# Kernel optimization log

Measured on AMD Instinct MI355X. Metric: run time of the kernel, lower is better.

## Reference

```python
import jax, jax.numpy as jnp
import numpy as np
from jax import lax

K = 32768          # queue size
C = 100            # num_classes == len(cls_num_list1)
B = 1024           # batch size (features.shape[0] - K)
D = 128            # embedding dim
ALPHA = 0.05; BETA = 1.0; GAMMA = 1.0; SUPT = 1.0
T = 0.07; BASE_T = 0.07   # base_temperature defaults to temperature
SMOOTH = 0.0; EPS = 1e-12


def setup_inputs() -> dict:
    key = jax.random.key(0)
    k1, k2, k3, k4 = jax.random.split(key, 4)
    features = jax.random.normal(k1, (B + K, D), dtype=jnp.float32)
    features = features / jnp.linalg.norm(features, axis=1, keepdims=True)  # contrastive feats are L2-normalized
    centers = jax.random.normal(k2, (C, D), dtype=jnp.float32)
    centers = centers / jnp.linalg.norm(centers, axis=1, keepdims=True)
    sup_logits = jax.random.normal(k3, (B, C), dtype=jnp.float32)
    labels = jax.random.randint(k4, (B + K,), 0, C, dtype=jnp.int32)
    return {"features": features, "sup_logits": sup_logits, "centers": centers, "labels": labels}


def _loss(features, sup_logits, centers, labels):
    f32 = features.dtype
    lab_c = jnp.arange(C, dtype=labels.dtype)
    lab1 = jnp.concatenate([labels[:B], lab_c])                 # [B+C]
    mask = (labels[:B, None] == labels[None, :]).astype(f32)    # [B, B+K]
    mask1 = (lab1[:B, None] == lab1[None, :]).astype(f32)       # [B, B+C]
    # class counts over batch+queue (batch_cls_count) and batch+centers (batch_cls_count1)
    cls_count = jnp.zeros((C,), f32).at[labels].add(1.0)
    cls_count1 = jnp.zeros((C,), f32).at[lab1].add(1.0)
    diag = jnp.arange(B)
    logits_mask = jnp.ones((B, B + K), f32).at[diag, diag].set(0.0)
    logits_mask1 = jnp.ones((B, B + C), f32).at[diag, diag].set(0.0)
    mask = mask * logits_mask
    mask1 = mask1 * logits_mask1

    # ---- branch 1: batch anchors vs [batch, class centers] ----
    feats1 = jnp.concatenate([features[:B], centers], axis=0)   # [B+C, D]
    logits1 = (features[:B] @ feats1.T) / T                     # [B, B+C]
    logits1 = logits1 - lax.stop_gradient(logits1.max(axis=1, keepdims=True))
    exp1 = jnp.exp(logits1) * logits_mask1
    w1 = cls_count1[lab1][None, :] - mask1                      # per-instance class weight
    denom1 = (exp1 / w1).sum(axis=1, keepdims=True)
    log_prob1 = logits1 - jnp.log(denom1 + EPS)
    loss1 = -jnp.mean((mask1 * log_prob1).sum(1) / mask1.sum(1))

    # ---- branch 2: [sup_logits, batch anchors vs batch+queue] ----
    adc = (features[:B] @ features.T) / T                       # [B, B+K]
    logits = jnp.concatenate([sup_logits / SUPT, adc], axis=1)  # [B, C+B+K] (self.weight is None)
    logits = logits - lax.stop_gradient(logits.max(axis=1, keepdims=True))
    one_hot = jax.nn.one_hot(labels[:B], C, dtype=f32)
    one_hot = SMOOTH / (C - 1) * (1.0 - one_hot) + (1.0 - SMOOTH) * one_hot
    mask_full = jnp.concatenate([one_hot * BETA, mask * ALPHA], axis=1)
    lmask_full = jnp.concatenate([jnp.ones((B, C), f32), GAMMA * logits_mask], axis=1)
    expl = jnp.exp(logits) * lmask_full
    lab_full = jnp.concatenate([lab_c, labels])                 # [C+B+K]
    w = cls_count[lab_full][None, :] - mask_full
    denom = (expl / w).sum(axis=1, keepdims=True)
    log_prob = logits - jnp.log(denom + EPS)
    loss2 = -(T / BASE_T) * jnp.mean((mask_full * log_prob).sum(1) / mask_full.sum(1))
    return loss1 + loss2


def reference(features, sup_logits, centers, labels):
    return _loss(features, sup_logits, centers, labels)
```

## Files before the change

### kernel.cpp

```cpp
#include <hip/hip_runtime.h>
#include <math.h>

#define KQ   32768
#define CC   100
#define BB   1024
#define DD   128
#define NTOT (BB + KQ)
#define CB_CENT 1056
#define NCB  1060
#define NHIST 33
#define NCG2 132
#define CG_SUP 141
#define NSL  141

#define INV_T  14.285714285714286f
#define K2E    20.609929f
#define ALPHA  0.05f
#define EPSV   1e-12f

typedef __attribute__((ext_vector_type(8)))  short          short8;
typedef __attribute__((ext_vector_type(8)))  unsigned short ushort8;
typedef __attribute__((ext_vector_type(16))) float          float16;

__device__ __forceinline__ unsigned short f2bf_rne(float f) {
    unsigned int u = __float_as_uint(f);
    return (unsigned short)((u + 0x7FFFu + ((u >> 16) & 1u)) >> 16);
}


__global__ __launch_bounds__(256) void prep_k(const float* __restrict__ feats,
                                              const float* __restrict__ centers,
                                              const int* __restrict__ labels,
                                              unsigned short* __restrict__ X2,
                                              int* __restrict__ cntP,
                                              int* __restrict__ cntB) {
    const int b = blockIdx.x, t = threadIdx.x;
    if (b >= NCB) {
        const int h = b - NCB;
        __shared__ int hA[CC], hB[CC];
        if (t < CC) { hA[t] = 0; hB[t] = 0; }
        __syncthreads();
        const int base = h * 1024;
#pragma unroll
        for (int q = 0; q < 4; ++q) {
            int l = labels[base + q * 256 + t];
            atomicAdd(&hA[l], 1);
            if (h == 0) atomicAdd(&hB[l], 1);
        }
        __syncthreads();
        if (t < 128) {
            cntP[h * 128 + t] = (t < CC) ? hA[t] : 0;
            if (h == 0) cntB[t] = (t < CC) ? hB[t] : 0;
        }
        return;
    }
    __shared__ unsigned short sm[8 * 66 * 8];
    const int cb = b;
    const int rl = t >> 3, c8 = t & 7;
    const int r = cb * 32 + rl;
    const float* src;
    if (r < NTOT)            src = &feats[(size_t)r * DD];
    else if (r < NTOT + CC)  src = &centers[(size_t)(r - NTOT) * DD];
    else                     src = nullptr;
#pragma unroll
    for (int s = 0; s < 2; ++s) {
        const int c8p = c8 + 8 * s;
        float v[8];
        if (src) {
            const float4* p = (const float4*)(src + c8p * 8);
            float4 q0 = p[0], q1 = p[1];
            v[0]=q0.x; v[1]=q0.y; v[2]=q0.z; v[3]=q0.w;
            v[4]=q1.x; v[5]=q1.y; v[6]=q1.z; v[7]=q1.w;
        } else {
#pragma unroll
            for (int j = 0; j < 8; ++j) v[j] = 0.f;
        }
        ushort8 H;
#pragma unroll
        for (int m = 0; m < 8; ++m) H[m] = f2bf_rne(v[m]);
        const int ks = c8p >> 1, lh = c8p & 1;
        *(ushort8*)&sm[(ks * 66 + rl + 32 * lh) * 8] = H;
    }
    __syncthreads();
    ushort8* dst = (ushort8*)((char*)X2 + (size_t)cb * 8192);
#pragma unroll
    for (int j = 0; j < 2; ++j) {
        const int idx = j * 256 + t;
        const int ks = idx >> 6, ln2 = idx & 63;
        dst[idx] = *(const ushort8*)&sm[(ks * 66 + ln2) * 8];
    }
}

__global__ __launch_bounds__(128) void tables_k(
    const int* __restrict__ cntP, const int* __restrict__ cntB,
    float2* __restrict__ wA, float2* __restrict__ w1, float2* __restrict__ wS,
    float* __restrict__ cAf, int* __restrict__ cBi) {
    const int t = threadIdx.x;
    int s = 0;
#pragma unroll
    for (int h = 0; h < NHIST; ++h) s += cntP[h * 128 + t];
    float cf = (float)s;
    float rn = (s > 0) ? __builtin_amdgcn_rcpf(cf) : 0.f;
    float dr = (s > 0) ? (__builtin_amdgcn_rcpf(cf - ALPHA) - rn) : 0.f;
    wA[t] = make_float2(rn, dr);
    wS[t] = make_float2(__builtin_amdgcn_rcpf(cf),
                        __builtin_amdgcn_rcpf(fmaxf(cf - 1.f, 1.f)));
    int sb = cntB[t];
    float c1 = (float)(sb + 1);
    float r1 = __builtin_amdgcn_rcpf(c1);
    w1[t] = make_float2(r1, __builtin_amdgcn_rcpf(fmaxf(c1 - 1.f, 1.f)) - r1);
    cAf[t] = cf;
    cBi[t] = sb;
}

__device__ __forceinline__ void epi_tile(
    const float16& acc, int cb, int lc, float rn, float drm, bool checkDiag,
    int half, int ln, int growbase, const int* rlab, float* sS, float* sN)
{
    const int ccol = cb * 32 + ln;
#pragma unroll
    for (int reg = 0; reg < 16; ++reg) {
        int ro = (reg & 3) + 8 * (reg >> 2) + 4 * half;
        float a  = acc[reg];
        float mf = (lc == rlab[reg]) ? 1.f : 0.f;
        float wgt = fmaf(mf, drm, rn);
        if (checkDiag) {
            bool d = (ccol == growbase + ro);
            wgt = d ? 0.f : wgt;
            mf  = d ? 0.f : mf;
        }
        float e = exp2f(fmaf(a, K2E, -K2E));
        sS[reg] = fmaf(e, wgt, sS[reg]);
        sN[reg] = fmaf(mf, a, sN[reg]);
    }
}

__global__ __launch_bounds__(256, 2) void gemm_k(
    const unsigned short* __restrict__ X2, const int* __restrict__ labels,
    const float2* __restrict__ wA, const float2* __restrict__ w1,
    const float2* __restrict__ wS, const float* __restrict__ sup,
    float* __restrict__ pS, float* __restrict__ pN,
    float* __restrict__ supS, float* __restrict__ supLi) {
    const int b = blockIdx.x;
    const int xcd = b & 7, rgrp = (b >> 3) & 7, chunk = b >> 6;
    const int cg = chunk * 8 + xcd;
    if (cg > CG_SUP) return;

    const int tid = threadIdx.x;
    const int w = tid >> 6, lane = tid & 63;
    const int half = lane >> 5, ln = lane & 31;
    const int rb = rgrp * 4 + w;
    const char* Xb = (const char*)X2;

    if (cg == CG_SUP) {
        const int c0 = lane, c1 = lane + 64;
        float2 t0 = wS[c0];
        float rA0 = t0.x, rAm0 = t0.y;
        float rA1 = 0.f, rAm1 = 0.f;
        if (lane < 36) { float2 t1v = wS[c1]; rA1 = t1v.x; rAm1 = t1v.y; }
        for (int rr = 0; rr < 32; ++rr) {
            int row = rb * 32 + rr;
            int li = labels[row];
            const float* srow = &sup[(size_t)row * CC];
            float v0 = srow[c0];
            float s = __expf(v0 - INV_T) * ((c0 == li) ? rAm0 : rA0);
            float liv = (c0 == li) ? v0 : 0.f;
            if (lane < 36) {
                float v1 = srow[c1];
                s += __expf(v1 - INV_T) * ((c1 == li) ? rAm1 : rA1);
                liv += (c1 == li) ? v1 : 0.f;
            }
#pragma unroll
            for (int off = 1; off < 64; off <<= 1) {
                s += __shfl_xor(s, off, 64);
                liv += __shfl_xor(liv, off, 64);
            }
            if (lane == 0) { supS[row] = s; supLi[row] = liv; }
        }
        return;
    }

    __shared__ char sm[2 * 8192];
    __shared__ float2 wT[128];

    const bool isB2 = (cg < NCG2);
    const int t1 = cg - NCG2;
    const bool isBatch = isB2 || (t1 < 8);
    const int NIT = isB2 ? 8 : 4;
    const int cb0 = isB2 ? cg * 8 : (t1 < 8 ? t1 * 4 : CB_CENT);

    if (tid < 128) wT[tid] = isB2 ? wA[tid] : w1[tid];
    __syncthreads();

    int lcv[8];
#pragma unroll
    for (int i = 0; i < 8; ++i) {
        if (i < NIT) {
            const int cb = cb0 + i;
            if (isBatch) {
                lcv[i] = labels[cb * 32 + ln];
            } else {
                int q = cb * 32 + ln - NTOT;
                lcv[i] = (q < CC) ? q : -1;
            }
        } else lcv[i] = -1;
    }

    const int growbase = rb * 32;
    short8 Ah[8];
    {
        size_t abase = (size_t)rb * 8192 + (size_t)lane * 16;
#pragma unroll
        for (int ks = 0; ks < 8; ++ks)
            Ah[ks] = *(const short8*)(Xb + abase + (size_t)ks * 1024);
    }
    int rlab[16];
#pragma unroll
    for (int reg = 0; reg < 16; ++reg) {
        int ro = (reg & 3) + 8 * (reg >> 2) + 4 * half;
        rlab[reg] = labels[growbase + ro];
    }

    float rnv[8], drv[8];
#pragma unroll
    for (int i = 0; i < 8; ++i) {
        if (i < NIT) {
            int lc = lcv[i];
            float2 wv = wT[(lc >= 0) ? lc : 0];
            rnv[i] = (lc >= 0) ? wv.x : 0.f;
            drv[i] = (lc >= 0) ? wv.y : 0.f;
        } else { rnv[i] = 0.f; drv[i] = 0.f; }
    }

    float sS[16], sN[16];
#pragma unroll
    for (int reg = 0; reg < 16; ++reg) { sS[reg] = 0.f; sN[reg] = 0.f; }

    const int soff = (w * 2) * 1024 + lane * 16;

    {
        const char* src = Xb + (size_t)cb0 * 8192 + soff;
        short8 s0 = *(const short8*)src;
        short8 s1 = *(const short8*)(src + 1024);
        *(short8*)&sm[soff] = s0;
        *(short8*)&sm[soff + 1024] = s1;
    }
    __syncthreads();

    for (int i = 0; i < NIT; ++i) {
        const int cb = cb0 + i;
        short8 st0, st1;
        const bool more = (i + 1 < NIT);
        if (more) {
            const char* src = Xb + (size_t)(cb + 1) * 8192 + soff;
            st0 = *(const short8*)src;
            st1 = *(const short8*)(src + 1024);
        }
        const char* Bp = &sm[(i & 1) * 8192 + lane * 16];
        float16 a;
#pragma unroll
        for (int reg = 0; reg < 16; ++reg) a[reg] = 0.f;
#pragma unroll
        for (int ks = 0; ks < 8; ++ks) {
            short8 Bf = *(const short8*)(Bp + ks * 1024);
            a = __builtin_amdgcn_mfma_f32_32x32x16_bf16(Ah[ks], Bf, a, 0, 0, 0);
        }
        epi_tile(a, cb, lcv[i], rnv[i], drv[i], isBatch && (cb == rb),
                 half, ln, growbase, rlab, sS, sN);
        if (more) {
            char* d = &sm[((i + 1) & 1) * 8192 + soff];
            *(short8*)d = st0;
            *(short8*)(d + 1024) = st1;
        }
        __syncthreads();
    }

    const int slice = isB2 ? cg : (NCG2 + t1);
#pragma unroll
    for (int reg = 0; reg < 16; ++reg) {
        float av = sS[reg], c = sN[reg];
#pragma unroll
        for (int off = 1; off < 32; off <<= 1) {
            av += __shfl_xor(av, off, 64);
            c  += __shfl_xor(c, off, 64);
        }
        if (ln == 0) {
            int ro = (reg & 3) + 8 * (reg >> 2) + 4 * half;
            int grow = growbase + ro;
            pS[(size_t)slice * BB + grow] = av;
            pN[(size_t)slice * BB + grow] = c;
        }
    }
}

__global__ __launch_bounds__(256) void reduce_k(
    const int* __restrict__ labels,
    const float* __restrict__ cAf, const int* __restrict__ cBi,
    const float* __restrict__ pS, const float* __restrict__ pN,
    const float* __restrict__ supS, const float* __restrict__ supLi,
    float* __restrict__ partial) {
    const int g = blockIdx.x, t = threadIdx.x;
    const int rl = t >> 5, j = t & 31;
    const int row = g * 8 + rl;
    float S2 = 0.f, N2 = 0.f, S1 = 0.f, N1v = 0.f;
    for (int c = j; c < NCG2; c += 32) {
        S2 += pS[(size_t)c * BB + row];
        N2 += pN[(size_t)c * BB + row];
    }
    if (NCG2 + j < NSL) {
        S1  += pS[(size_t)(NCG2 + j) * BB + row];
        N1v += pN[(size_t)(NCG2 + j) * BB + row];
    }
#pragma unroll
    for (int off = 1; off < 32; off <<= 1) {
        S2 += __shfl_xor(S2, off, 64);  N2  += __shfl_xor(N2, off, 64);
        S1 += __shfl_xor(S1, off, 64);  N1v += __shfl_xor(N1v, off, 64);
    }
    float s = 0.f;
    if (j == 0) {
        int li = labels[row];
        S2 += supS[row];
        N2 *= INV_T; N1v *= INV_T;
        float sli = supLi[row];
        float cA = cAf[li];
        float msum2 = fmaf(ALPHA, cA - 1.f, 1.f);
        float loss2 = -(fmaf(ALPHA, N2, sli) / msum2 - INV_T - logf(S2 + EPSV));
        float loss1 = -(N1v / (float)cBi[li] - INV_T - logf(S1 + EPSV));
        s = loss1 + loss2;
    }
#pragma unroll
    for (int off = 1; off < 64; off <<= 1) s += __shfl_xor(s, off, 64);
    __shared__ float buf[4];
    if ((t & 63) == 0) buf[t >> 6] = s;
    __syncthreads();
    if (t == 0) partial[g] = (buf[0] + buf[1]) + (buf[2] + buf[3]);
}

__global__ __launch_bounds__(64) void final_k(const float* __restrict__ partial,
                                              float* __restrict__ out) {
    const int t = threadIdx.x;
    float s = partial[t] + partial[t + 64];
#pragma unroll
    for (int off = 1; off < 64; off <<= 1) s += __shfl_xor(s, off, 64);
    if (t == 0) out[0] = s / (float)BB;
}

extern "C" void kernel_launch(void* const* d_in, const int* in_sizes, int n_in,
                              void* d_out, int out_size, void* d_ws, size_t ws_size,
                              hipStream_t stream) {
    const float* feats   = (const float*)d_in[0];
    const float* sup     = (const float*)d_in[1];
    const float* centers = (const float*)d_in[2];
    const int*   labels  = (const int*)d_in[3];
    float* out = (float*)d_out;
    char*  wsb = (char*)d_ws;

    const size_t X2_BYTES = (size_t)NCB * 8192;
    unsigned short* X2 = (unsigned short*)wsb;
    char* base2 = wsb + X2_BYTES;
    int* cntP = (int*)base2;
    int* cntB = cntP + NHIST * 128;
    float2* wA = (float2*)(cntB + 128);
    float2* w1 = wA + 128;
    float2* wS = w1 + 128;
    float*  cAf = (float*)(wS + 128);
    int*    cBi = (int*)(cAf + 128);
    float* pS = (float*)(cBi + 128);
    float* pN = pS + (size_t)NSL * BB;
    float* supS  = pN + (size_t)NSL * BB;
    float* supLi = supS + BB;
    float* partial = supLi + BB;

    prep_k<<<NCB + NHIST, 256, 0, stream>>>(feats, centers, labels, X2, cntP, cntB);
    tables_k<<<1, 128, 0, stream>>>(cntP, cntB, wA, w1, wS, cAf, cBi);
    gemm_k<<<18 * 64, 256, 0, stream>>>(X2, labels, wA, w1, wS, sup,
                                        pS, pN, supS, supLi);
    reduce_k<<<128, 256, 0, stream>>>(labels, cAf, cBi, pS, pN, supS, supLi, partial);
    final_k<<<1, 64, 0, stream>>>(partial, out);
}
```

Baseline: 121.5 us.

## Give each wave two 32-row A tiles to double reuse of staged B tiles

Each wave now holds two 32-row anchor blocks in registers and runs two MFMA chains against every shared-memory column tile, so each block covers 256 rows and the grid shrinks from 1152 to 576 blocks. The aim is to halve how often the queue feature tiles are loaded from global memory and copied into LDS. The cost is roughly double the register footprint (A fragments, accumulators, label and sum arrays) under launch_bounds(256,2), which can cause spills or lower occupancy, and there are half as many blocks to spread across CUs. The sup-logit path is rescaled to 64 rows per wave to match the new grid.

After: 153.8 us. 1.27x slower.

```diff
diff --git a/kernel.cpp b/kernel.cpp
--- a/kernel.cpp
+++ b/kernel.cpp
@@ -142,14 +142,13 @@
     float* __restrict__ pS, float* __restrict__ pN,
     float* __restrict__ supS, float* __restrict__ supLi) {
     const int b = blockIdx.x;
-    const int xcd = b & 7, rgrp = (b >> 3) & 7, chunk = b >> 6;
+    const int xcd = b & 7, rgrp = (b >> 3) & 3, chunk = b >> 5;
     const int cg = chunk * 8 + xcd;
     if (cg > CG_SUP) return;
 
     const int tid = threadIdx.x;
     const int w = tid >> 6, lane = tid & 63;
     const int half = lane >> 5, ln = lane & 31;
-    const int rb = rgrp * 4 + w;
     const char* Xb = (const char*)X2;
 
     if (cg == CG_SUP) {
@@ -158,8 +157,9 @@
         float rA0 = t0.x, rAm0 = t0.y;
         float rA1 = 0.f, rAm1 = 0.f;
         if (lane < 36) { float2 t1v = wS[c1]; rA1 = t1v.x; rAm1 = t1v.y; }
-        for (int rr = 0; rr < 32; ++rr) {
-            int row = rb * 32 + rr;
+        const int rbase = rgrp * 256 + w * 64;
+        for (int rr = 0; rr < 64; ++rr) {
+            int row = rbase + rr;
             int li = labels[row];
             const float* srow = &sup[(size_t)row * CC];
             float v0 = srow[c0];
@@ -190,7 +190,9 @@
     const int cb0 = isB2 ? cg * 8 : (t1 < 8 ? t1 * 4 : CB_CENT);
 
     if (tid < 128) wT[tid] = isB2 ? wA[tid] : w1[tid];
-    __syncthreads();
+
+    const int rb0 = rgrp * 8 + w * 2, rb1 = rb0 + 1;
+    const int growb0 = rb0 * 32, growb1 = rb1 * 32;
 
     int lcv[8];
 #pragma unroll
@@ -206,35 +208,29 @@
         } else lcv[i] = -1;
     }
 
-    const int growbase = rb * 32;
-    short8 Ah[8];
+    short8 Ah0[8], Ah1[8];
     {
-        size_t abase = (size_t)rb * 8192 + (size_t)lane * 16;
-#pragma unroll
-        for (int ks = 0; ks < 8; ++ks)
-            Ah[ks] = *(const short8*)(Xb + abase + (size_t)ks * 1024);
-    }
-    int rlab[16];
+        size_t a0 = (size_t)rb0 * 8192 + (size_t)lane * 16;
+        size_t a1 = (size_t)rb1 * 8192 + (size_t)lane * 16;
+#pragma unroll
+        for (int ks = 0; ks < 8; ++ks) {
+            Ah0[ks] = *(const short8*)(Xb + a0 + (size_t)ks * 1024);
+            Ah1[ks] = *(const short8*)(Xb + a1 + (size_t)ks * 1024);
+        }
+    }
+    int rlab0[16], rlab1[16];
 #pragma unroll
     for (int reg = 0; reg < 16; ++reg) {
         int ro = (reg & 3) + 8 * (reg >> 2) + 4 * half;
-        rlab[reg] = labels[growbase + ro];
-    }
-
-    float rnv[8], drv[8];
-#pragma unroll
-    for (int i = 0; i < 8; ++i) {
-        if (i < NIT) {
-            int lc = lcv[i];
-            float2 wv = wT[(lc >= 0) ? lc : 0];
-            rnv[i] = (lc >= 0) ? wv.x : 0.f;
-            drv[i] = (lc >= 0) ? wv.y : 0.f;
-        } else { rnv[i] = 0.f; drv[i] = 0.f; }
-    }
-
-    float sS[16], sN[16];
-#pragma unroll
-    for (int reg = 0; reg < 16; ++reg) { sS[reg] = 0.f; sN[reg] = 0.f; }
+        rlab0[reg] = labels[growb0 + ro];
+        rlab1[reg] = labels[growb1 + ro];
+    }
+
+    float sS0[16], sN0[16], sS1[16], sN1[16];
+#pragma unroll
+    for (int reg = 0; reg < 16; ++reg) {
+        sS0[reg] = 0.f; sN0[reg] = 0.f; sS1[reg] = 0.f; sN1[reg] = 0.f;
+    }
 
     const int soff = (w * 2) * 1024 + lane * 16;
 
@@ -256,17 +252,24 @@
             st0 = *(const short8*)src;
             st1 = *(const short8*)(src + 1024);
         }
+        int lc = lcv[i];
+        float2 wv = wT[(lc >= 0) ? lc : 0];
+        float rn  = (lc >= 0) ? wv.x : 0.f;
+        float drm = (lc >= 0) ? wv.y : 0.f;
         const char* Bp = &sm[(i & 1) * 8192 + lane * 16];
-        float16 a;
-#pragma unroll
-        for (int reg = 0; reg < 16; ++reg) a[reg] = 0.f;
+        float16 a0, a1;
+#pragma unroll
+        for (int reg = 0; reg < 16; ++reg) { a0[reg] = 0.f; a1[reg] = 0.f; }
 #pragma unroll
         for (int ks = 0; ks < 8; ++ks) {
             short8 Bf = *(const short8*)(Bp + ks * 1024);
-            a = __builtin_amdgcn_mfma_f32_32x32x16_bf16(Ah[ks], Bf, a, 0, 0, 0);
-        }
-        epi_tile(a, cb, lcv[i], rnv[i], drv[i], isBatch && (cb == rb),
-                 half, ln, growbase, rlab, sS, sN);
+            a0 = __builtin_amdgcn_mfma_f32_32x32x16_bf16(Ah0[ks], Bf, a0, 0, 0, 0);
+            a1 = __builtin_amdgcn_mfma_f32_32x32x16_bf16(Ah1[ks], Bf, a1, 0, 0, 0);
+        }
+        epi_tile(a0, cb, lc, rn, drm, isBatch && (cb == rb0),
+                 half, ln, growb0, rlab0, sS0, sN0);
+        epi_tile(a1, cb, lc, rn, drm, isBatch && (cb == rb1),
+                 half, ln, growb1, rlab1, sS1, sN1);
         if (more) {
             char* d = &sm[((i + 1) & 1) * 8192 + soff];
             *(short8*)d = st0;
@@ -278,17 +281,21 @@
     const int slice = isB2 ? cg : (NCG2 + t1);
 #pragma unroll
     for (int reg = 0; reg < 16; ++reg) {
-        float av = sS[reg], c = sN[reg];
+        float av0 = sS0[reg], c0v = sN0[reg];
+        float av1 = sS1[reg], c1v = sN1[reg];
 #pragma unroll
         for (int off = 1; off < 32; off <<= 1) {
-            av += __shfl_xor(av, off, 64);
-            c  += __shfl_xor(c, off, 64);
+            av0 += __shfl_xor(av0, off, 64);
+            c0v += __shfl_xor(c0v, off, 64);
+            av1 += __shfl_xor(av1, off, 64);
+            c1v += __shfl_xor(c1v, off, 64);
         }
         if (ln == 0) {
             int ro = (reg & 3) + 8 * (reg >> 2) + 4 * half;
-            int grow = growbase + ro;
-            pS[(size_t)slice * BB + grow] = av;
-            pN[(size_t)slice * BB + grow] = c;
+            pS[(size_t)slice * BB + growb0 + ro] = av0;
+            pN[(size_t)slice * BB + growb0 + ro] = c0v;
+            pS[(size_t)slice * BB + growb1 + ro] = av1;
+            pN[(size_t)slice * BB + growb1 + ro] = c1v;
         }
     }
 }
@@ -373,7 +380,7 @@
 
     prep_k<<<NCB + NHIST, 256, 0, stream>>>(feats, centers, labels, X2, cntP, cntB);
     tables_k<<<1, 128, 0, stream>>>(cntP, cntB, wA, w1, wS, cAf, cBi);
-    gemm_k<<<18 * 64, 256, 0, stream>>>(X2, labels, wA, w1, wS, sup,
+    gemm_k<<<18 * 32, 256, 0, stream>>>(X2, labels, wA, w1, wS, sup,
                                         pS, pN, supS, supLi);
     reduce_k<<<128, 256, 0, stream>>>(labels, cAf, cBi, pS, pN, supS, supLi, partial);
     final_k<<<1, 64, 0, stream>>>(partial, out);
```

## Fold tables kernel into gemm/reduce and stage B tiles via global_load_lds

Applied to the files above, without the earlier changes.

Removes the single-block tables_k launch by having each gemm and reduce block recompute the class-count weight tables from the histogram partials. Replaces the register-staged global-to-LDS double-buffer copy with direct global_load_lds async loads, so the prefetch no longer holds VGPRs or needs explicit LDS stores. This saves one kernel launch and serialization gap, at the cost of redundant histogram summation in every block. It also relies on the async LDS writes being complete before the barrier without an explicit vmcnt wait.

New measurement: 121.1 us. No clear change (-0.3%).

```diff
diff --git a/kernel.cpp b/kernel.cpp
--- a/kernel.cpp
+++ b/kernel.cpp
@@ -25,6 +25,12 @@
 __device__ __forceinline__ unsigned short f2bf_rne(float f) {
     unsigned int u = __float_as_uint(f);
     return (unsigned short)((u + 0x7FFFu + ((u >> 16) & 1u)) >> 16);
+}
+
+__device__ __forceinline__ void glds16(const void* g, void* l) {
+    __builtin_amdgcn_global_load_lds(
+        (const __attribute__((address_space(1))) void*)g,
+        (__attribute__((address_space(3))) void*)l, 16, 0, 0);
 }
 
 
@@ -91,28 +97,6 @@
     }
 }
 
-__global__ __launch_bounds__(128) void tables_k(
-    const int* __restrict__ cntP, const int* __restrict__ cntB,
-    float2* __restrict__ wA, float2* __restrict__ w1, float2* __restrict__ wS,
-    float* __restrict__ cAf, int* __restrict__ cBi) {
-    const int t = threadIdx.x;
-    int s = 0;
-#pragma unroll
-    for (int h = 0; h < NHIST; ++h) s += cntP[h * 128 + t];
-    float cf = (float)s;
-    float rn = (s > 0) ? __builtin_amdgcn_rcpf(cf) : 0.f;
-    float dr = (s > 0) ? (__builtin_amdgcn_rcpf(cf - ALPHA) - rn) : 0.f;
-    wA[t] = make_float2(rn, dr);
-    wS[t] = make_float2(__builtin_amdgcn_rcpf(cf),
-                        __builtin_amdgcn_rcpf(fmaxf(cf - 1.f, 1.f)));
-    int sb = cntB[t];
-    float c1 = (float)(sb + 1);
-    float r1 = __builtin_amdgcn_rcpf(c1);
-    w1[t] = make_float2(r1, __builtin_amdgcn_rcpf(fmaxf(c1 - 1.f, 1.f)) - r1);
-    cAf[t] = cf;
-    cBi[t] = sb;
-}
-
 __device__ __forceinline__ void epi_tile(
     const float16& acc, int cb, int lc, float rn, float drm, bool checkDiag,
     int half, int ln, int growbase, const int* rlab, float* sS, float* sN)
@@ -137,8 +121,8 @@
 
 __global__ __launch_bounds__(256, 2) void gemm_k(
     const unsigned short* __restrict__ X2, const int* __restrict__ labels,
-    const float2* __restrict__ wA, const float2* __restrict__ w1,
-    const float2* __restrict__ wS, const float* __restrict__ sup,
+    const int* __restrict__ cntP, const int* __restrict__ cntB,
+    const float* __restrict__ sup,
     float* __restrict__ pS, float* __restrict__ pN,
     float* __restrict__ supS, float* __restrict__ supLi) {
     const int b = blockIdx.x;
@@ -154,10 +138,21 @@
 
     if (cg == CG_SUP) {
         const int c0 = lane, c1 = lane + 64;
-        float2 t0 = wS[c0];
-        float rA0 = t0.x, rAm0 = t0.y;
+        int s0 = 0, s1 = 0;
+#pragma unroll
+        for (int h = 0; h < NHIST; ++h) {
+            s0 += cntP[h * 128 + c0];
+            s1 += cntP[h * 128 + c1];
+        }
+        float n0 = (float)s0;
+        float rA0 = __builtin_amdgcn_rcpf(n0);
+        float rAm0 = __builtin_amdgcn_rcpf(fmaxf(n0 - 1.f, 1.f));
         float rA1 = 0.f, rAm1 = 0.f;
-        if (lane < 36) { float2 t1v = wS[c1]; rA1 = t1v.x; rAm1 = t1v.y; }
+        if (lane < 36) {
+            float n1 = (float)s1;
+            rA1 = __builtin_amdgcn_rcpf(n1);
+            rAm1 = __builtin_amdgcn_rcpf(fmaxf(n1 - 1.f, 1.f));
+        }
         for (int rr = 0; rr < 32; ++rr) {
             int row = rb * 32 + rr;
             int li = labels[row];
@@ -189,8 +184,29 @@
     const int NIT = isB2 ? 8 : 4;
     const int cb0 = isB2 ? cg * 8 : (t1 < 8 ? t1 * 4 : CB_CENT);
 
-    if (tid < 128) wT[tid] = isB2 ? wA[tid] : w1[tid];
-    __syncthreads();
+    if (tid < 128) {
+        int s = 0;
+#pragma unroll
+        for (int h = 0; h < NHIST; ++h) s += cntP[h * 128 + tid];
+        float2 wv;
+        if (isB2) {
+            float cf = (float)s;
+            float rn = (s > 0) ? __builtin_amdgcn_rcpf(cf) : 0.f;
+            wv = make_float2(rn, (s > 0) ? (__builtin_amdgcn_rcpf(cf - ALPHA) - rn) : 0.f);
+        } else {
+            float c1 = (float)(cntB[tid] + 1);
+            float r1 = __builtin_amdgcn_rcpf(c1);
+            wv = make_float2(r1, __builtin_amdgcn_rcpf(fmaxf(c1 - 1.f, 1.f)) - r1);
+        }
+        wT[tid] = wv;
+    }
+
+    const int wbase = w * 2048;
+    {
+        const char* src = Xb + (size_t)cb0 * 8192 + wbase + lane * 16;
+        glds16(src, &sm[wbase]);
+        glds16(src + 1024, &sm[wbase + 1024]);
+    }
 
     int lcv[8];
 #pragma unroll
@@ -221,6 +237,8 @@
         rlab[reg] = labels[growbase + ro];
     }
 
+    __syncthreads();
+
     float rnv[8], drv[8];
 #pragma unroll
     for (int i = 0; i < 8; ++i) {
@@ -236,25 +254,14 @@
 #pragma unroll
     for (int reg = 0; reg < 16; ++reg) { sS[reg] = 0.f; sN[reg] = 0.f; }
 
-    const int soff = (w * 2) * 1024 + lane * 16;
-
-    {
-        const char* src = Xb + (size_t)cb0 * 8192 + soff;
-        short8 s0 = *(const short8*)src;
-        short8 s1 = *(const short8*)(src + 1024);
-        *(short8*)&sm[soff] = s0;
-        *(short8*)&sm[soff + 1024] = s1;
-    }
-    __syncthreads();
-
     for (int i = 0; i < NIT; ++i) {
         const int cb = cb0 + i;
-        short8 st0, st1;
         const bool more = (i + 1 < NIT);
         if (more) {
-            const char* src = Xb + (size_t)(cb + 1) * 8192 + soff;
-            st0 = *(const short8*)src;
-            st1 = *(const short8*)(src + 1024);
+            const char* src = Xb + (size_t)(cb + 1) * 8192 + wbase + lane * 16;
+            char* dl = &sm[((i + 1) & 1) * 8192 + wbase];
+            glds16(src, dl);
+            glds16(src + 1024, dl + 1024);
         }
         const char* Bp = &sm[(i & 1) * 8192 + lane * 16];
         float16 a;
@@ -267,11 +274,6 @@
         }
         epi_tile(a, cb, lcv[i], rnv[i], drv[i], isBatch && (cb == rb),
                  half, ln, growbase, rlab, sS, sN);
-        if (more) {
-            char* d = &sm[((i + 1) & 1) * 8192 + soff];
-            *(short8*)d = st0;
-            *(short8*)(d + 1024) = st1;
-        }
         __syncthreads();
     }
 
@@ -295,11 +297,21 @@
 
 __global__ __launch_bounds__(256) void reduce_k(
     const int* __restrict__ labels,
-    const float* __restrict__ cAf, const int* __restrict__ cBi,
+    const int* __restrict__ cntP, const int* __restrict__ cntB,
     const float* __restrict__ pS, const float* __restrict__ pN,
     const float* __restrict__ supS, const float* __restrict__ supLi,
     float* __restrict__ partial) {
     const int g = blockIdx.x, t = threadIdx.x;
+    __shared__ float cA_s[128];
+    __shared__ int   cB_s[128];
+    if (t < 128) {
+        int s = 0;
+#pragma unroll
+        for (int h = 0; h < NHIST; ++h) s += cntP[h * 128 + t];
+        cA_s[t] = (float)s;
+        cB_s[t] = cntB[t];
+    }
+    __syncthreads();
     const int rl = t >> 5, j = t & 31;
     const int row = g * 8 + rl;
     float S2 = 0.f, N2 = 0.f, S1 = 0.f, N1v = 0.f;
@@ -322,10 +334,10 @@
         S2 += supS[row];
         N2 *= INV_T; N1v *= INV_T;
         float sli = supLi[row];
-        float cA = cAf[li];
+        float cA = cA_s[li];
         float msum2 = fmaf(ALPHA, cA - 1.f, 1.f);
         float loss2 = -(fmaf(ALPHA, N2, sli) / msum2 - INV_T - logf(S2 + EPSV));
-        float loss1 = -(N1v / (float)cBi[li] - INV_T - logf(S1 + EPSV));
+        float loss1 = -(N1v / (float)cB_s[li] - INV_T - logf(S1 + EPSV));
         s = loss1 + loss2;
     }
 #pragma unroll
@@ -360,21 +372,15 @@
     char* base2 = wsb + X2_BYTES;
     int* cntP = (int*)base2;
     int* cntB = cntP + NHIST * 128;
-    float2* wA = (float2*)(cntB + 128);
-    float2* w1 = wA + 128;
-    float2* wS = w1 + 128;
-    float*  cAf = (float*)(wS + 128);
-    int*    cBi = (int*)(cAf + 128);
-    float* pS = (float*)(cBi + 128);
+    float* pS = (float*)(cntB + 128);
     float* pN = pS + (size_t)NSL * BB;
     float* supS  = pN + (size_t)NSL * BB;
     float* supLi = supS + BB;
     float* partial = supLi + BB;
 
     prep_k<<<NCB + NHIST, 256, 0, stream>>>(feats, centers, labels, X2, cntP, cntB);
-    tables_k<<<1, 128, 0, stream>>>(cntP, cntB, wA, w1, wS, cAf, cBi);
-    gemm_k<<<18 * 64, 256, 0, stream>>>(X2, labels, wA, w1, wS, sup,
+    gemm_k<<<18 * 64, 256, 0, stream>>>(X2, labels, cntP, cntB, sup,
                                         pS, pN, supS, supLi);
-    reduce_k<<<128, 256, 0, stream>>>(labels, cAf, cBi, pS, pN, supS, supLi, partial);
+    reduce_k<<<128, 256, 0, stream>>>(labels, cntP, cntB, pS, pN, supS, supLi, partial);
     final_k<<<1, 64, 0, stream>>>(partial, out);
 }
```
